# Kernel tuning notes

Measured on AMD Instinct MI355X. Metric: run time of the kernel, lower is better.

The kernel has to match this reference:

```python
import jax, jax.numpy as jnp
import numpy as np

N, E, G = 50000, 800000, 512          # nodes, edges, graphs in batch
DIN, DH, H, DOUT = 128, 128, 2, 128   # dim_in, dim_h, heads, dim_out
NEG_SLOPE = 0.2
EPS_BN = 1e-5


def setup_inputs():
    key = jax.random.key(0)
    ks = jax.random.split(key, 12)
    def glorot(k, shape, fan):
        return (jax.random.normal(k, shape, jnp.float32) / np.float32(np.sqrt(fan)))
    return dict(
        x=jax.random.normal(ks[0], (N, DIN), jnp.float32),
        edge_index=jax.random.randint(ks[1], (2, E), 0, N, dtype=jnp.int32),
        batch=jnp.sort(jax.random.randint(ks[2], (N,), 0, G, dtype=jnp.int32)),
        Wl1=glorot(ks[3], (DIN, H * DH), DIN),
        Wr1=glorot(ks[4], (DIN, H * DH), DIN),
        att1=glorot(ks[5], (H, DH), DH),
        b1=jnp.zeros((H * DH,), jnp.float32),
        gamma=jnp.ones((H * DH,), jnp.float32),
        beta=jnp.zeros((H * DH,), jnp.float32),
        Wl2=glorot(ks[6], (H * DH, DOUT), H * DH),
        Wr2=glorot(ks[7], (H * DH, DOUT), H * DH),
        att2=glorot(ks[8], (1, DOUT), DOUT),
        b2=jnp.zeros((DOUT,), jnp.float32),
        Wlin=glorot(ks[9], (DOUT, 2), DOUT),
        blin=jnp.zeros((2,), jnp.float32),
    )


def gatv2_conv(x, src, dst, Wl, Wr, att, bias, heads, dh, n):
    # x: [n, F]; src/dst: [Etot] (self-loops already appended)
    xl = (x @ Wl).reshape(n, heads, dh)  # source transform (messages)
    xr = (x @ Wr).reshape(n, heads, dh)  # target transform
    m = xl[src] + xr[dst]                             # [Etot, H, dh]
    e = jnp.einsum('ehd,hd->eh', jax.nn.leaky_relu(m, NEG_SLOPE), att)  # [Etot, H]
    # softmax over incoming edges of each target node
    emax = jax.ops.segment_max(e, dst, num_segments=n)
    ex = jnp.exp(e - emax[dst])
    denom = jax.ops.segment_sum(ex, dst, num_segments=n)
    alpha = ex / (denom[dst] + 1e-16)                 # [Etot, H]
    out = jax.ops.segment_sum(xl[src] * alpha[:, :, None], dst, num_segments=n)
    return out.reshape(n, heads * dh) + bias


def reference(x, edge_index, batch, Wl1, Wr1, att1, b1, gamma, beta,
              Wl2, Wr2, att2, b2, Wlin, blin):
    loops = jnp.arange(N, dtype=edge_index.dtype)
    src = jnp.concatenate([edge_index[0], loops])
    dst = jnp.concatenate([edge_index[1], loops])

    h = gatv2_conv(x, src, dst, Wl1, Wr1, att1, b1, H, DH, N)   # [N, H*DH]
    h = jax.nn.elu(h)
    # BatchNorm over node dimension (training-mode batch stats)
    mu = h.mean(axis=0)
    var = h.var(axis=0)
    h = (h - mu) * jax.lax.rsqrt(var + EPS_BN) * gamma + beta
    # dropout p=0 -> identity
    h = gatv2_conv(h, src, dst, Wl2, Wr2, att2, b2, 1, DOUT, N)  # [N, DOUT]

    # global mean pool per graph
    s = jax.ops.segment_sum(h, batch, num_segments=G)
    cnt = jax.ops.segment_sum(jnp.ones((N,), h.dtype), batch, num_segments=G)
    pooled = s / jnp.maximum(cnt, 1.0)[:, None]                  # [G, DOUT]
    return pooled @ Wlin + blin                                  # [G, 2]
```

## Files before the change

kernel.cpp:

```cpp
#include <hip/hip_runtime.h>


#define DIN 128
#define F1 256
#define F2 128
#define NEG_SLOPE 0.2f

typedef unsigned short u16;
typedef __attribute__((ext_vector_type(8))) short short8;
typedef __attribute__((ext_vector_type(4))) float floatx4;

__device__ __forceinline__ float bf2f(u16 u) {
  return __uint_as_float(((unsigned int)u) << 16);
}
__device__ __forceinline__ u16 f2bf(float f) {
  unsigned int x = __float_as_uint(f);
  return (u16)((x + 0x7fffu + ((x >> 16) & 1u)) >> 16);
}
__device__ __forceinline__ void load8(const u16* p, float (&f)[8]) {
  short8 v = *(const short8*)p;
#pragma unroll
  for (int k = 0; k < 8; k++) f[k] = bf2f((u16)v[k]);
}

struct PTab { const void* src[8]; int off[9]; };
__global__ __launch_bounds__(256) void k_convert_all(
    const void* __restrict__ xsrc, u16* __restrict__ xb, int n4, int nxb,
    PTab t, u16* __restrict__ pb, int ptotal, int npb,
    const void* __restrict__ Wl1s, const void* __restrict__ Wr1s,
    const void* __restrict__ Wl2s, const void* __restrict__ Wr2s,
    u16* __restrict__ Wl1t, u16* __restrict__ Wr1t,
    u16* __restrict__ Wl2t, u16* __restrict__ Wr2t,
    int* __restrict__ zbase, int zn, int* __restrict__ flag) {
  __shared__ int flagS;
  int tid = threadIdx.x;
  if (tid < 64) {
    int cnt = 0;
#pragma unroll
    for (int i = 0; i < 2; ++i) {
      u16 v = ((const u16*)xsrc)[2 * (tid + 64 * i)];
      int e = (v >> 7) & 0xFF;
      if (e >= 115 && e <= 130) cnt++;
    }
#pragma unroll
    for (int m = 1; m <= 32; m <<= 1) cnt += __shfl_xor(cnt, m, 64);
    if (tid == 0) flagS = (cnt < 64) ? 1 : 0;
  }
  __syncthreads();
  const int fl = flagS;
  if (blockIdx.x == 0 && tid == 0) *flag = fl;

  int b = blockIdx.x;
  if (b < nxb) {
    int i = b * 256 + tid;
    if (i >= n4) return;
    if (fl) {
      float4 a = ((const float4*)xsrc)[i];
      ushort4 o;
      o.x = f2bf(a.x); o.y = f2bf(a.y); o.z = f2bf(a.z); o.w = f2bf(a.w);
      ((ushort4*)xb)[i] = o;
    } else {
      ((ulong1*)xb)[i] = ((const ulong1*)xsrc)[i];
    }
    return;
  }
  b -= nxb;
  if (b < npb) {
    int i = b * 256 + tid;
    if (i >= ptotal) return;
    int s = 0;
#pragma unroll
    for (int k = 1; k < 8; k++) s += (i >= t.off[k]);
    int local = i - t.off[s];
    pb[i] = fl ? f2bf(((const float*)t.src[s])[local]) : ((const u16*)t.src[s])[local];
    return;
  }
  b -= npb;
  if (b < 512) {
    int seg = b >> 7;
    int i = (b & 127) * 256 + tid;
    const void* s; u16* d; int NL, sh;
    if      (seg == 0) { s = Wl1s; d = Wl1t; NL = 256; sh = 7; }
    else if (seg == 1) { s = Wr1s; d = Wr1t; NL = 256; sh = 7; }
    else if (seg == 2) { s = Wl2s; d = Wl2t; NL = 128; sh = 8; }
    else               { s = Wr2s; d = Wr2t; NL = 128; sh = 8; }
    int n = i >> sh, k = i & ((1 << sh) - 1);
    int si = k * NL + n;
    d[i] = fl ? f2bf(((const float*)s)[si]) : ((const u16*)s)[si];
    return;
  }
  b -= 512;
  int i = b * 256 + tid;
  if (i < zn) zbase[i] = 0;
}

__global__ void k_hist(const int* __restrict__ ei, int* __restrict__ hist,
                       int E, int Etot) {
  int e = blockIdx.x * 256 + threadIdx.x;
  if (e >= Etot) return;
  int dst = (e < E) ? ei[E + e] : (e - E);
  atomicAdd(&hist[dst], 1);
}

__global__ void k_scan(const int* __restrict__ hist, int* __restrict__ rowptr,
                       int* __restrict__ cursor, unsigned long long* __restrict__ pstate,
                       int* __restrict__ ctr, int n, int Etot) {
  __shared__ int tmp[256];
  __shared__ int bidS, offS;
  int t = threadIdx.x;
  if (t == 0) bidS = atomicAdd(ctr, 1);
  __syncthreads();
  int bid = bidS;
  int gid = bid * 256 + t;
  int v = (gid < n) ? hist[gid] : 0;
  tmp[t] = v;
  __syncthreads();
  for (int off = 1; off < 256; off <<= 1) {
    int add = (t >= off) ? tmp[t - off] : 0;
    __syncthreads();
    tmp[t] += add;
    __syncthreads();
  }
  if (t == 0) {
    int total = tmp[255];
    unsigned long long st =
        ((unsigned long long)(bid == 0 ? 2 : 1) << 32) | (unsigned)total;
    atomicExch(&pstate[bid], st);
    int off = 0;
    if (bid > 0) {
      int b = bid - 1;
      while (true) {
        unsigned long long s;
        do { s = atomicAdd(&pstate[b], 0ULL); } while ((s >> 32) == 0);
        off += (int)(unsigned)s;
        if ((s >> 32) == 2) break;
        b--;
      }
      atomicExch(&pstate[bid],
                 ((unsigned long long)2 << 32) | (unsigned)(off + total));
    }
    offS = off;
  }
  __syncthreads();
  int off = offS;
  if (gid < n) {
    int ex = off + tmp[t] - v;
    rowptr[gid] = ex;
    cursor[gid] = ex;
  }
  if (gid == 0) rowptr[n] = Etot;
}

__global__ void k_scatter(const int* __restrict__ ei, int* __restrict__ cursor,
                          int* __restrict__ ssrc, int E, int Etot) {
  int e = blockIdx.x * 256 + threadIdx.x;
  if (e >= Etot) return;
  int src, dst;
  if (e < E) { src = ei[e]; dst = ei[E + e]; }
  else       { src = e - E; dst = e - E; }
  int pos = atomicAdd(&cursor[dst], 1);
  ssrc[pos] = src;
}

template<int K, bool RB>
__global__ __launch_bounds__(256) void k_gemm(
    const u16* __restrict__ A, const u16* __restrict__ Blt, const u16* __restrict__ Brt,
    int NL, u16* __restrict__ Cl, u16* __restrict__ Cr, int M,
    const float* __restrict__ rbias) {
  const int tid = threadIdx.x;
  const int m0 = blockIdx.x * 64;
  const int n0g = blockIdx.y * 64;
  const u16* Bt; u16* C; int col0;
  if (n0g < NL) { Bt = Blt; C = Cl; col0 = n0g; }
  else          { Bt = Brt; C = Cr; col0 = n0g - NL; }

  const int wave = tid >> 6, lane = tid & 63;
  const int wm = wave >> 1, wn = wave & 1;
  const int quad = lane >> 4, l16 = lane & 15;

  floatx4 acc[2][2] = {};
#pragma unroll
  for (int k0 = 0; k0 < K; k0 += 32) {
    short8 af[2], bfr[2];
#pragma unroll
    for (int mt = 0; mt < 2; mt++) {
      int row = m0 + wm * 32 + mt * 16 + l16;
      if (row > M - 1) row = M - 1;
      af[mt] = *(const short8*)(A + (size_t)row * K + k0 + quad * 8);
    }
#pragma unroll
    for (int nt = 0; nt < 2; nt++) {
      int nn = col0 + wn * 32 + nt * 16 + l16;
      bfr[nt] = *(const short8*)(Bt + (size_t)nn * K + k0 + quad * 8);
    }
#pragma unroll
    for (int mt = 0; mt < 2; mt++)
#pragma unroll
      for (int nt = 0; nt < 2; nt++)
        acc[mt][nt] = __builtin_amdgcn_mfma_f32_16x16x32_bf16(af[mt], bfr[nt], acc[mt][nt], 0, 0, 0);
  }

#pragma unroll
  for (int mt = 0; mt < 2; mt++)
#pragma unroll
    for (int nt = 0; nt < 2; nt++) {
      float rb = 0.f;
      if (RB) rb = rbias[n0g + wn * 32 + nt * 16 + l16];
#pragma unroll
      for (int r = 0; r < 4; r++) {
        int row = m0 + wm * 32 + mt * 16 + quad * 4 + r;
        if (row < M) {
          int col = col0 + wn * 32 + nt * 16 + l16;
          C[(size_t)row * NL + col] = f2bf(acc[mt][nt][r] + rb);
        }
      }
    }
}

template<int HEADS, int MODE>
__global__ __launch_bounds__(256) void k_agg(
    const u16* __restrict__ xl, const u16* __restrict__ xr,
    const u16* __restrict__ att, const u16* __restrict__ bias,
    const int* __restrict__ rowptr, const int* __restrict__ ssrc,
    void* __restrict__ outv, int n) {
  constexpr int F = HEADS * 128;
  constexpr int EPI = 4 / HEADS;
  int wave = threadIdx.x >> 6, lane = threadIdx.x & 63;
  int node = blockIdx.x * 4 + wave;
  if (node >= n) return;
  const int q = lane >> 4, l = lane & 15;
  const int eo   = (HEADS == 2) ? (q >> 1) : q;
  const int head = (HEADS == 2) ? (q & 1) : 0;
  const int ch0 = head * 128 + l * 8;

  float xrv[8], attv[8], acc[8];
  load8(xr + (size_t)node * F + ch0, xrv);
  load8(att + ch0, attv);
#pragma unroll
  for (int k = 0; k < 8; k++) acc[k] = 0.f;

  float l_run = 0.f;
  const int jb = rowptr[node], je = rowptr[node + 1];
  for (int j = jb; j < je; j += EPI) {
    int jj = j + eo;
    int src = ssrc[jj < je ? jj : (je - 1)];
    float xlv[8];
    load8(xl + (size_t)src * F + ch0, xlv);
    float s = 0.f;
#pragma unroll
    for (int k = 0; k < 8; k++) {
      float mm = xlv[k] + xrv[k];
      mm = mm > 0.f ? mm : NEG_SLOPE * mm;
      s += mm * attv[k];
    }
#pragma unroll
    for (int m = 1; m <= 8; m <<= 1) s += __shfl_xor(s, m, 64);
    float p = (jj < je) ? __expf(fminf(s, 80.f)) : 0.f;
    l_run += p;
#pragma unroll
    for (int k = 0; k < 8; k++) acc[k] += p * xlv[k];
  }

#pragma unroll
  for (int m = 16 * HEADS; m <= 32; m <<= 1) {
#pragma unroll
    for (int k = 0; k < 8; k++) acc[k] += __shfl_xor(acc[k], m, 64);
    l_run += __shfl_xor(l_run, m, 64);
  }

  if (lane < 16 * HEADS) {
    float inv = 1.f / (l_run + 1e-16f);
    if (MODE == 0) {
      short8 o;
#pragma unroll
      for (int k = 0; k < 8; k++) {
        float t = acc[k] * inv + bf2f(bias[ch0 + k]);
        t = t > 0.f ? t : (__expf(t) - 1.f);
        o[k] = (short)f2bf(t);
      }
      *(short8*)((u16*)outv + (size_t)node * F + ch0) = o;
    } else {
      float v[8];
#pragma unroll
      for (int k = 0; k < 8; k++) v[k] = acc[k] * inv + bf2f(bias[ch0 + k]);
      float* op = (float*)outv + (size_t)node * F + ch0;
      *(float4*)op = make_float4(v[0], v[1], v[2], v[3]);
      *(float4*)(op + 4) = make_float4(v[4], v[5], v[6], v[7]);
    }
  }
}

__global__ __launch_bounds__(256) void k_stats(
    const u16* __restrict__ h, float* __restrict__ gsum,
    float* __restrict__ gsumsq, int n) {
  __shared__ float smS[8][256], smQ[8][256];
  int t = threadIdx.x;
  int rg = t >> 5, cl = t & 31;
  int ch0 = cl * 8;
  float s[8] = {}, q[8] = {};
  for (int r = blockIdx.x * 8 + rg; r < n; r += gridDim.x * 8) {
    float v[8];
    load8(h + (size_t)r * F1 + ch0, v);
#pragma unroll
    for (int k = 0; k < 8; k++) { s[k] += v[k]; q[k] += v[k] * v[k]; }
  }
#pragma unroll
  for (int k = 0; k < 8; k++) { smS[rg][ch0 + k] = s[k]; smQ[rg][ch0 + k] = q[k]; }
  __syncthreads();
  float ts = 0.f, tq = 0.f;
#pragma unroll
  for (int g = 0; g < 8; g++) { ts += smS[g][t]; tq += smQ[g][t]; }
  atomicAdd(&gsum[t], ts);
  atomicAdd(&gsumsq[t], tq);
}

__global__ __launch_bounds__(256) void k_foldbn(
    const float* __restrict__ gsum, const float* __restrict__ gsumsq,
    const u16* __restrict__ gamma, const u16* __restrict__ beta,
    u16* __restrict__ Wl2t, u16* __restrict__ Wr2t,
    float* __restrict__ rbias, float invn) {
  __shared__ float red[8];
  int t = threadIdx.x, n = blockIdx.x;
  float mu = gsum[t] * invn;
  float var = gsumsq[t] * invn - mu * mu;
  float a = bf2f(gamma[t]) * rsqrtf(fmaxf(var, 0.f) + 1e-5f);
  float b = bf2f(beta[t]) - mu * a;
  float wl = bf2f(Wl2t[n * 256 + t]);
  float wr = bf2f(Wr2t[n * 256 + t]);
  float sl = b * wl, sr = b * wr;
  Wl2t[n * 256 + t] = f2bf(a * wl);
  Wr2t[n * 256 + t] = f2bf(a * wr);
#pragma unroll
  for (int m = 1; m <= 32; m <<= 1) {
    sl += __shfl_xor(sl, m, 64);
    sr += __shfl_xor(sr, m, 64);
  }
  int wave = t >> 6, lane = t & 63;
  if (lane == 0) { red[wave] = sl; red[4 + wave] = sr; }
  __syncthreads();
  if (t == 0) rbias[n] = red[0] + red[1] + red[2] + red[3];
  if (t == 1) rbias[128 + n] = red[4] + red[5] + red[6] + red[7];
}

__device__ __forceinline__ int lowerb(const int* __restrict__ a, int n, int key) {
  int lo = 0, hi = n;
  while (lo < hi) { int m = (lo + hi) >> 1; if (a[m] < key) lo = m + 1; else hi = m; }
  return lo;
}

__global__ __launch_bounds__(256) void k_poolfinal(
    const float* __restrict__ h2, const int* __restrict__ batch,
    const u16* __restrict__ Wlin, const u16* __restrict__ blin,
    void* __restrict__ out, const int* __restrict__ flag, int G, int N) {
  __shared__ float sm[4][128];
  int g = blockIdx.x;
  int wave = threadIdx.x >> 6, lane = threadIdx.x & 63;
  int jb = lowerb(batch, N, g);
  int je = lowerb(batch, N, g + 1);
  int ch = lane * 2;
  float c0 = 0.f, c1 = 0.f;
  for (int r = jb + wave; r < je; r += 4) {
    float2 v = *(const float2*)(h2 + (size_t)r * F2 + ch);
    c0 += v.x; c1 += v.y;
  }
  sm[wave][ch] = c0;
  sm[wave][ch + 1] = c1;
  __syncthreads();
  if (wave == 0) {
    c0 = sm[0][ch] + sm[1][ch] + sm[2][ch] + sm[3][ch];
    c1 = sm[0][ch + 1] + sm[1][ch + 1] + sm[2][ch + 1] + sm[3][ch + 1];
    float cf = fmaxf((float)(je - jb), 1.f);
    c0 /= cf; c1 /= cf;
    float s0 = c0 * bf2f(Wlin[ch * 2 + 0]) + c1 * bf2f(Wlin[(ch + 1) * 2 + 0]);
    float s1 = c0 * bf2f(Wlin[ch * 2 + 1]) + c1 * bf2f(Wlin[(ch + 1) * 2 + 1]);
#pragma unroll
    for (int m = 1; m <= 32; m <<= 1) {
      s0 += __shfl_xor(s0, m, 64);
      s1 += __shfl_xor(s1, m, 64);
    }
    if (lane == 0) {
      float o0 = s0 + bf2f(blin[0]);
      float o1 = s1 + bf2f(blin[1]);
      if (*flag) {
        ((float*)out)[g * 2 + 0] = o0;
        ((float*)out)[g * 2 + 1] = o1;
      } else {
        ((u16*)out)[g * 2 + 0] = f2bf(o0);
        ((u16*)out)[g * 2 + 1] = f2bf(o1);
      }
    }
  }
}

extern "C" void kernel_launch(void* const* d_in, const int* in_sizes, int n_in,
                              void* d_out, int out_size, void* d_ws, size_t ws_size,
                              hipStream_t stream) {
  const int* ei    = (const int*)d_in[1];
  const int* batch = (const int*)d_in[2];

  const int N = in_sizes[0] / DIN;
  const int E = in_sizes[1] / 2;
  const int G = out_size / 2;
  const int Etot = E + N;

  char* p = (char*)d_ws;
  auto alloc = [&](size_t bytes) {
    char* r = p;
    p += (bytes + 255) & ~(size_t)255;
    return r;
  };
  int*  flag     = (int*)alloc(256);
  int*  hist     = (int*)alloc((size_t)N * 4);
  float* gsum    = (float*)alloc(1024);
  float* gsumsq  = (float*)alloc(1024);
  unsigned long long* pstate = (unsigned long long*)alloc(2048);
  int*  ctr      = (int*)alloc(256);
  int   zn       = (int)(((char*)ctr + 256) - (char*)hist) / 4;
  int*  rowptr   = (int*)alloc((size_t)(N + 1) * 4);
  int*  cursor   = (int*)alloc((size_t)N * 4);
  float* rbias   = (float*)alloc(256 * 4);
  int*  ssrc     = (int*)alloc((size_t)Etot * 4);
  u16*  xb       = (u16*)alloc((size_t)N * DIN * 2);
  u16*  pb       = (u16*)alloc(4096);
  u16*  Wl1t     = (u16*)alloc(DIN * F1 * 2);
  u16*  Wr1t     = (u16*)alloc(DIN * F1 * 2);
  u16*  Wl2t     = (u16*)alloc(F1 * F2 * 2);
  u16*  Wr2t     = (u16*)alloc(F1 * F2 * 2);
  u16*  regionA  = (u16*)alloc((size_t)N * F1 * 2);
  u16*  regionB  = (u16*)alloc((size_t)N * F1 * 2);
  u16*  regionC  = (u16*)alloc((size_t)N * F1 * 2);

  u16*  xl1  = regionA;
  u16*  xr1  = regionB;
  u16*  helu = regionC;
  u16*  xl2  = regionB;
  u16*  xr2  = regionB + (size_t)N * F2;
  float* h2  = (float*)regionA;

  const int pidx[8] = {5, 6, 7, 8, 11, 12, 13, 14};
  PTab tab;
  int accum = 0;
  for (int i = 0; i < 8; i++) {
    tab.src[i] = d_in[pidx[i]];
    tab.off[i] = accum;
    accum += in_sizes[pidx[i]];
  }
  tab.off[8] = accum;
  int n4 = in_sizes[0] / 4;
  int nxb = (n4 + 255) / 256;
  int npb = (accum + 255) / 256;
  int nzb = (zn + 255) / 256;
  k_convert_all<<<nxb + npb + 512 + nzb, 256, 0, stream>>>(
      d_in[0], xb, n4, nxb, tab, pb, accum, npb,
      d_in[3], d_in[4], d_in[9], d_in[10], Wl1t, Wr1t, Wl2t, Wr2t,
      hist, zn, flag);
  u16 *pAtt1 = pb + tab.off[0], *pB1 = pb + tab.off[1], *pGamma = pb + tab.off[2],
      *pBeta = pb + tab.off[3], *pAtt2 = pb + tab.off[4], *pB2 = pb + tab.off[5],
      *pWlin = pb + tab.off[6], *pBlin = pb + tab.off[7];

  const int eb = (Etot + 255) / 256;
  const int sb = (N + 255) / 256;

  k_hist<<<eb, 256, 0, stream>>>(ei, hist, E, Etot);
  k_scan<<<sb, 256, 0, stream>>>(hist, rowptr, cursor, pstate, ctr, N, Etot);
  k_scatter<<<eb, 256, 0, stream>>>(ei, cursor, ssrc, E, Etot);

  dim3 g1((N + 63) / 64, (2 * F1) / 64);
  k_gemm<DIN, false><<<g1, 256, 0, stream>>>(xb, Wl1t, Wr1t, F1, xl1, xr1, N, nullptr);

  k_agg<2, 0><<<(N + 3) / 4, 256, 0, stream>>>(xl1, xr1, pAtt1, pB1, rowptr, ssrc, helu, N);

  k_stats<<<256, 256, 0, stream>>>(helu, gsum, gsumsq, N);
  k_foldbn<<<128, 256, 0, stream>>>(gsum, gsumsq, pGamma, pBeta, Wl2t, Wr2t, rbias,
                                    1.0f / (float)N);

  dim3 g2((N + 63) / 64, (2 * F2) / 64);
  k_gemm<F1, true><<<g2, 256, 0, stream>>>(helu, Wl2t, Wr2t, F2, xl2, xr2, N, rbias);

  k_agg<1, 1><<<(N + 3) / 4, 256, 0, stream>>>(xl2, xr2, pAtt2, pB2, rowptr, ssrc, h2, N);

  k_poolfinal<<<G, 256, 0, stream>>>(h2, batch, pWlin, pBlin, d_out, flag, G, N);
}
```

Baseline: 454.2 us.

## Restructure GAT aggregation: wider per-lane channels, DPP reductions, gather prefetch

The aggregation kernel now gives each lane a contiguous run of 8 or 16 channels, so every quarter-wave handles a whole edge row and four edges are processed per iteration for both layers. The first layer previously processed only two edges per iteration. The xl row gather for the next batch of edges is software-prefetched into registers while the current batch is being computed. The attention-logit reduction uses DPP lane permutes instead of shuffles. The cost is higher register pressure from 16-float arrays plus prefetch buffers, which may lower occupancy.

```diff
diff --git a/kernel.cpp b/kernel.cpp
--- a/kernel.cpp
+++ b/kernel.cpp
@@ -21,6 +21,17 @@
   short8 v = *(const short8*)p;
 #pragma unroll
   for (int k = 0; k < 8; k++) f[k] = bf2f((u16)v[k]);
+}
+__device__ __forceinline__ void load8p(const u16* p, float* f) {
+  short8 v = *(const short8*)p;
+#pragma unroll
+  for (int k = 0; k < 8; k++) f[k] = bf2f((u16)v[k]);
+}
+
+template <int CTRL>
+__device__ __forceinline__ float dppadd(float s) {
+  int t = __builtin_amdgcn_update_dpp(0, __float_as_int(s), CTRL, 0xF, 0xF, false);
+  return s + __int_as_float(t);
 }
 
 struct PTab { const void* src[8]; int off[9]; };
@@ -217,75 +228,108 @@
     }
 }
 
-template<int HEADS, int MODE>
+template<int CPL, int MODE>
 __global__ __launch_bounds__(256) void k_agg(
     const u16* __restrict__ xl, const u16* __restrict__ xr,
     const u16* __restrict__ att, const u16* __restrict__ bias,
     const int* __restrict__ rowptr, const int* __restrict__ ssrc,
     void* __restrict__ outv, int n) {
-  constexpr int F = HEADS * 128;
-  constexpr int EPI = 4 / HEADS;
+  constexpr int F = CPL * 16;
+  constexpr int NV = CPL / 8;
   int wave = threadIdx.x >> 6, lane = threadIdx.x & 63;
   int node = blockIdx.x * 4 + wave;
   if (node >= n) return;
   const int q = lane >> 4, l = lane & 15;
-  const int eo   = (HEADS == 2) ? (q >> 1) : q;
-  const int head = (HEADS == 2) ? (q & 1) : 0;
-  const int ch0 = head * 128 + l * 8;
-
-  float xrv[8], attv[8], acc[8];
-  load8(xr + (size_t)node * F + ch0, xrv);
-  load8(att + ch0, attv);
-#pragma unroll
-  for (int k = 0; k < 8; k++) acc[k] = 0.f;
-
+  const int ch0 = l * CPL;
+
+  float xrv[CPL], attv[CPL], acc[CPL];
+#pragma unroll
+  for (int v = 0; v < NV; v++) {
+    load8p(xr + (size_t)node * F + ch0 + v * 8, &xrv[v * 8]);
+    load8p(att + ch0 + v * 8, &attv[v * 8]);
+  }
+#pragma unroll
+  for (int c = 0; c < CPL; c++) acc[c] = 0.f;
+
+  const int jb = rowptr[node], je = rowptr[node + 1];
   float l_run = 0.f;
-  const int jb = rowptr[node], je = rowptr[node + 1];
-  for (int j = jb; j < je; j += EPI) {
-    int jj = j + eo;
-    int src = ssrc[jj < je ? jj : (je - 1)];
-    float xlv[8];
-    load8(xl + (size_t)src * F + ch0, xlv);
+
+  int jj = jb + q;
+  int scur = ssrc[jj < je ? jj : je - 1];
+  int jn = jb + 4 + q;
+  int snxt = ssrc[jn < je ? jn : je - 1];
+  short8 cur[NV], nxt[NV];
+#pragma unroll
+  for (int v = 0; v < NV; v++)
+    cur[v] = *(const short8*)(xl + (size_t)scur * F + ch0 + v * 8);
+
+  for (int j = jb; j < je; j += 4) {
+#pragma unroll
+    for (int v = 0; v < NV; v++)
+      nxt[v] = *(const short8*)(xl + (size_t)snxt * F + ch0 + v * 8);
+    int jnn = j + 8 + q;
+    snxt = ssrc[jnn < je ? jnn : je - 1];
+
+    float xlv[CPL];
+#pragma unroll
+    for (int v = 0; v < NV; v++)
+#pragma unroll
+      for (int k = 0; k < 8; k++) xlv[v * 8 + k] = bf2f((u16)cur[v][k]);
+
     float s = 0.f;
 #pragma unroll
-    for (int k = 0; k < 8; k++) {
-      float mm = xlv[k] + xrv[k];
-      mm = mm > 0.f ? mm : NEG_SLOPE * mm;
-      s += mm * attv[k];
-    }
-#pragma unroll
-    for (int m = 1; m <= 8; m <<= 1) s += __shfl_xor(s, m, 64);
-    float p = (jj < je) ? __expf(fminf(s, 80.f)) : 0.f;
+    for (int c = 0; c < CPL; c++) {
+      float m = xlv[c] + xrv[c];
+      m = m > 0.f ? m : NEG_SLOPE * m;
+      s += m * attv[c];
+    }
+    s = dppadd<0xB1>(s);
+    s = dppadd<0x4E>(s);
+    s = dppadd<0x141>(s);
+    if (CPL == 8) s = dppadd<0x140>(s);
+
+    float p = (j + q < je) ? __expf(fminf(s, 80.f)) : 0.f;
     l_run += p;
 #pragma unroll
-    for (int k = 0; k < 8; k++) acc[k] += p * xlv[k];
-  }
-
-#pragma unroll
-  for (int m = 16 * HEADS; m <= 32; m <<= 1) {
-#pragma unroll
-    for (int k = 0; k < 8; k++) acc[k] += __shfl_xor(acc[k], m, 64);
-    l_run += __shfl_xor(l_run, m, 64);
-  }
-
-  if (lane < 16 * HEADS) {
+    for (int c = 0; c < CPL; c++) acc[c] += p * xlv[c];
+
+#pragma unroll
+    for (int v = 0; v < NV; v++) cur[v] = nxt[v];
+  }
+
+#pragma unroll
+  for (int c = 0; c < CPL; c++) {
+    acc[c] += __shfl_xor(acc[c], 16, 64);
+    acc[c] += __shfl_xor(acc[c], 32, 64);
+  }
+  l_run += __shfl_xor(l_run, 16, 64);
+  l_run += __shfl_xor(l_run, 32, 64);
+
+  if (q == 0) {
     float inv = 1.f / (l_run + 1e-16f);
     if (MODE == 0) {
-      short8 o;
-#pragma unroll
-      for (int k = 0; k < 8; k++) {
-        float t = acc[k] * inv + bf2f(bias[ch0 + k]);
-        t = t > 0.f ? t : (__expf(t) - 1.f);
-        o[k] = (short)f2bf(t);
+#pragma unroll
+      for (int v = 0; v < NV; v++) {
+        short8 o;
+#pragma unroll
+        for (int k = 0; k < 8; k++) {
+          float t = acc[v * 8 + k] * inv + bf2f(bias[ch0 + v * 8 + k]);
+          t = t > 0.f ? t : (__expf(t) - 1.f);
+          o[k] = (short)f2bf(t);
+        }
+        *(short8*)((u16*)outv + (size_t)node * F + ch0 + v * 8) = o;
       }
-      *(short8*)((u16*)outv + (size_t)node * F + ch0) = o;
     } else {
-      float v[8];
-#pragma unroll
-      for (int k = 0; k < 8; k++) v[k] = acc[k] * inv + bf2f(bias[ch0 + k]);
-      float* op = (float*)outv + (size_t)node * F + ch0;
-      *(float4*)op = make_float4(v[0], v[1], v[2], v[3]);
-      *(float4*)(op + 4) = make_float4(v[4], v[5], v[6], v[7]);
+#pragma unroll
+      for (int v = 0; v < NV; v++) {
+        float w[8];
+#pragma unroll
+        for (int k = 0; k < 8; k++)
+          w[k] = acc[v * 8 + k] * inv + bf2f(bias[ch0 + v * 8 + k]);
+        float* op = (float*)outv + (size_t)node * F + ch0 + v * 8;
+        *(float4*)op = make_float4(w[0], w[1], w[2], w[3]);
+        *(float4*)(op + 4) = make_float4(w[4], w[5], w[6], w[7]);
+      }
     }
   }
 }
@@ -468,7 +512,7 @@
   dim3 g1((N + 63) / 64, (2 * F1) / 64);
   k_gemm<DIN, false><<<g1, 256, 0, stream>>>(xb, Wl1t, Wr1t, F1, xl1, xr1, N, nullptr);
 
-  k_agg<2, 0><<<(N + 3) / 4, 256, 0, stream>>>(xl1, xr1, pAtt1, pB1, rowptr, ssrc, helu, N);
+  k_agg<16, 0><<<(N + 3) / 4, 256, 0, stream>>>(xl1, xr1, pAtt1, pB1, rowptr, ssrc, helu, N);
 
   k_stats<<<256, 256, 0, stream>>>(helu, gsum, gsumsq, N);
   k_foldbn<<<128, 256, 0, stream>>>(gsum, gsumsq, pGamma, pBeta, Wl2t, Wr2t, rbias,
@@ -477,7 +521,7 @@
   dim3 g2((N + 63) / 64, (2 * F2) / 64);
   k_gemm<F1, true><<<g2, 256, 0, stream>>>(helu, Wl2t, Wr2t, F2, xl2, xr2, N, rbias);
 
-  k_agg<1, 1><<<(N + 3) / 4, 256, 0, stream>>>(xl2, xr2, pAtt2, pB2, rowptr, ssrc, h2, N);
+  k_agg<8, 1><<<(N + 3) / 4, 256, 0, stream>>>(xl2, xr2, pAtt2, pB2, rowptr, ssrc, h2, N);
 
   k_poolfinal<<<G, 256, 0, stream>>>(h2, batch, pWlin, pBlin, d_out, flag, G, N);
 }
```

Result: no change. 459.0 us (+1.0%).
